# Optimization experiments

Measured on AMD Instinct MI355X. Metric: run time of the kernel, lower is better.

The kernel has to match this reference:

```python
import jax, jax.numpy as jnp
import numpy as np

B, L, D, H = 8, 2048, 1024, 1024
BASE_LR, BASE_WD = 0.01, 0.9


def setup_inputs() -> dict:
    key = jax.random.key(0)
    ks = jax.random.split(key, 8)
    s = 1.0 / np.sqrt(D)
    return {
        "x": jax.random.normal(ks[0], (B, L, D), jnp.float32),
        "hidden": jax.random.normal(ks[1], (B, D, H), jnp.float32),
        "log_base_lr": jnp.array([np.log(BASE_LR)], jnp.float32),
        "w_lr": jax.random.normal(ks[2], (D, 1), jnp.float32) * s,
        "b_lr": jnp.zeros((1,), jnp.float32),
        "log_base_wd": jnp.array([np.log(BASE_WD)], jnp.float32),
        "w_wd": jax.random.normal(ks[3], (D, 1), jnp.float32) * s,
        "b_wd": jnp.zeros((1,), jnp.float32),
        "w_q": jax.random.normal(ks[4], (D, H), jnp.float32) * s,
        "b_q": jnp.zeros((H,), jnp.float32),
        "w_k": jax.random.normal(ks[5], (D, H), jnp.float32) * s,
        "b_k": jnp.zeros((H,), jnp.float32),
        "w_v": jax.random.normal(ks[6], (D, D), jnp.float32) * s,
        "b_v": jnp.zeros((D,), jnp.float32),
    }


def reference(x, hidden, log_base_lr, w_lr, b_lr, log_base_wd, w_wd, b_wd,
              w_q, b_q, w_k, b_k, w_v, b_v):
    batch, length, dim = x.shape
    W_prev = hidden  # [b, d, h]
    query = x @ w_q + b_q                     # [b, l, h]
    key = x @ w_k + b_k                       # [b, l, h]
    value = x @ w_v + b_v                     # [b, l, d]
    lr = jnp.exp(log_base_lr) * jax.nn.sigmoid((x @ w_lr + b_lr)[..., 0])  # [b, l]
    # log(1 - base_wd * sigmoid(.)) via log1p for stability; same math.
    log_wd = jnp.log1p(-jnp.exp(log_base_wd) * jax.nn.sigmoid((x @ w_wd + b_wd)[..., 0]))  # [b, l]
    wd_cross = jnp.exp(jnp.cumsum(log_wd, axis=1))  # [b, l]
    # inner-chunk decay: entry [b, m, l] = exp(sum_{j=m+1..l} log_wd[b, j]) for l >= m
    tri = jnp.triu(jnp.broadcast_to(log_wd[:, None, :], (batch, length, length)), k=1)
    wd_inner = jnp.triu(jnp.exp(jnp.cumsum(tri, axis=2)))  # [b, l, l]
    kq = jnp.einsum('bld,bmd->blm', key, query)            # [b, l, m]
    mask_kq = kq * wd_inner
    WpK_V = jnp.einsum('bdh,blh->bld', W_prev, key) - value  # [b, l, d]
    y_inner = -jnp.einsum('bld,bl,blm->bmd', WpK_V, lr, mask_kq)
    y_cross = jnp.einsum('bdh,blh,bl->bld', W_prev, query, wd_cross)
    y = y_inner + y_cross
    W_next_inner = -jnp.einsum('bld,bl,blh->bdh', WpK_V, lr * wd_inner[:, :, -1], key)
    W_next_cross = W_prev * wd_cross[:, -1][:, None, None]
    W_next = W_next_inner + W_next_cross
    return y, W_next
```

## Files before the change

### kernel.cpp

```cpp
#include <hip/hip_runtime.h>
#include <stdint.h>

#define BB 8
#define LL 2048
#define DD 1024
#define HH 1024
#define BL (BB*LL)

typedef __attribute__((ext_vector_type(8))) short short8;
typedef __attribute__((ext_vector_type(4))) float f32x4;

__device__ __forceinline__ unsigned short f2bf(float f) {
  unsigned int x = __float_as_uint(f);
  unsigned int r = (x + 0x7fffu + ((x >> 16) & 1u)) >> 16;
  return (unsigned short)r;
}
__device__ __forceinline__ float bf2f(unsigned short u) {
  return __uint_as_float(((unsigned int)u) << 16);
}

__device__ __forceinline__ void stage16(const unsigned short* g, unsigned short* l) {
  __builtin_amdgcn_global_load_lds((const __attribute__((address_space(1))) void*)g,
                                   (__attribute__((address_space(3))) void*)l,
                                   16, 0, 0);
}

struct __align__(16) Smem8 {
  unsigned short a[2][16384];
  unsigned short b[2][16384];
};
static_assert(sizeof(Smem8) == 131072, "LDS size");

__device__ __forceinline__ void acc_init8(f32x4 (&acc)[8][4]) {
#pragma unroll
  for (int i = 0; i < 8; ++i)
#pragma unroll
    for (int j = 0; j < 4; ++j)
      acc[i][j] = (f32x4){0.f, 0.f, 0.f, 0.f};
}

template<class FA, class FB>
__device__ __forceinline__ void gemm8_core(FA srcA, FB srcB, int NK,
                                           Smem8* sm, f32x4 (&acc)[8][4]) {
  const int lane = threadIdx.x & 63;
  const int wave = threadIdx.x >> 6;
  const int srow = lane >> 3;
  const int scol = ((lane & 7) ^ srow) * 8;
  const int fk = (lane >> 4) * 8;
  const int fr = lane & 15;
  const int fx = fr & 7;
  const int mwr = (wave >> 2) * 128;
  const int nwr = (wave & 3) * 64;
  const int cA0 = (wave < 4) ? 2 * wave : 2 * wave + 8;
  const int cA1 = cA0 + 8;
  const int cB0 = (wave >> 1) * 8 + 2 * (wave & 1);
  const int cB1 = cB0 + 4;

  auto SA = [&](int p, int kt, int c) {
    stage16(srcA(c * 8 + srow, kt) + scol, &sm->a[p][c * 512]);
    stage16(srcA(c * 8 + 8 + srow, kt) + scol, &sm->a[p][(c + 1) * 512]);
  };
  auto SB = [&](int p, int kt, int c) {
    stage16(srcB(c * 8 + srow, kt) + scol, &sm->b[p][c * 512]);
    stage16(srcB(c * 8 + 8 + srow, kt) + scol, &sm->b[p][(c + 1) * 512]);
  };
  const int kc0 = (((fk >> 3) ^ fx) << 3);
  const int kc1 = ((((32 + fk) >> 3) ^ fx) << 3);

  short8 af[4], bfv[4][2];
  auto LDBk = [&](int p, int kk, int kc) {
#pragma unroll
    for (int j = 0; j < 4; ++j)
      bfv[j][kk] = *(const short8*)&sm->b[p][(nwr + j * 16 + fr) * 64 + kc];
  };
  auto LDA4 = [&](int p, int ih, int kc) {
#pragma unroll
    for (int i = 0; i < 4; ++i)
      af[i] = *(const short8*)&sm->a[p][(mwr + ih * 64 + i * 16 + fr) * 64 + kc];
  };
  auto MMk = [&](int ih, int kk) {
#pragma unroll
    for (int i = 0; i < 4; ++i)
#pragma unroll
      for (int j = 0; j < 4; ++j)
        acc[ih * 4 + i][j] = __builtin_amdgcn_mfma_f32_16x16x32_bf16(
            af[i], bfv[j][kk], acc[ih * 4 + i][j], 0, 0, 0);
  };

#define SCB  __builtin_amdgcn_sched_barrier(0)
#define BARB __builtin_amdgcn_s_barrier()
#define LGKM0 do { asm volatile("s_waitcnt lgkmcnt(0)" ::: "memory"); SCB; } while (0)

  SA(0, 0, cA0); SA(0, 0, cA1); SB(0, 0, cB0); SB(0, 0, cB1);
  asm volatile("s_waitcnt vmcnt(0)" ::: "memory");
  SCB; BARB; SCB;

  for (int t = 0; t < NK; ++t) {
    const int p = t & 1, po = p ^ 1;
    const bool s1 = (t + 1 < NK);
    LDA4(p, 0, kc0); LDBk(p, 0, kc0);
    if (s1) { SA(po, t + 1, cA0); SA(po, t + 1, cA1); }
    SCB; BARB; LGKM0;
    __builtin_amdgcn_s_setprio(1); MMk(0, 0); __builtin_amdgcn_s_setprio(0);
    SCB; BARB; SCB;
    LDA4(p, 1, kc0);
    if (s1) { SB(po, t + 1, cB0); SB(po, t + 1, cB1); }
    SCB; BARB; LGKM0;
    __builtin_amdgcn_s_setprio(1); MMk(1, 0); __builtin_amdgcn_s_setprio(0);
    SCB; BARB; SCB;
    LDA4(p, 0, kc1); LDBk(p, 1, kc1);
    SCB; BARB; LGKM0;
    __builtin_amdgcn_s_setprio(1); MMk(0, 1); __builtin_amdgcn_s_setprio(0);
    SCB; BARB; SCB;
    LDA4(p, 1, kc1);
    SCB; BARB; LGKM0;
    __builtin_amdgcn_s_setprio(1); MMk(1, 1); __builtin_amdgcn_s_setprio(0);
    SCB;
    if (s1) { asm volatile("s_waitcnt vmcnt(0)" ::: "memory"); }
    SCB; BARB; SCB;
  }
#undef LGKM0
#undef BARB
#undef SCB
}

template<typename F>
__device__ __forceinline__ void epi8(const f32x4 (&acc)[8][4], F body) {
  const int lane = threadIdx.x & 63;
  const int wave = threadIdx.x >> 6;
  const int mwr = (wave >> 2) * 128, nwr = (wave & 3) * 64;
#pragma unroll
  for (int i = 0; i < 8; ++i)
#pragma unroll
    for (int j = 0; j < 4; ++j)
#pragma unroll
      for (int jj = 0; jj < 4; ++jj)
        body(mwr + i * 16 + ((lane >> 4) << 2) + jj,
             nwr + j * 16 + (lane & 15), acc[i][j][jj]);
}


__global__ void k_prep_x(const float* __restrict__ x, const float* __restrict__ wlr,
                         const float* __restrict__ wwd, unsigned short* __restrict__ xb,
                         float* __restrict__ lrlog, float* __restrict__ wdlog) {
  const int wave = threadIdx.x >> 6, lane = threadIdx.x & 63;
  const int row = blockIdx.x * 4 + wave;
  const float* xr = x + (size_t)row * DD;
  float s1 = 0.f, s2 = 0.f;
#pragma unroll
  for (int ch = 0; ch < 4; ++ch) {
    const int col = ch * 256 + lane * 4;
    float4 v = *(const float4*)(xr + col);
    float4 a = *(const float4*)(wlr + col);
    float4 b = *(const float4*)(wwd + col);
    s1 += v.x*a.x + v.y*a.y + v.z*a.z + v.w*a.w;
    s2 += v.x*b.x + v.y*b.y + v.z*b.z + v.w*b.w;
    uint2 u;
    u.x = (unsigned)f2bf(v.x) | ((unsigned)f2bf(v.y) << 16);
    u.y = (unsigned)f2bf(v.z) | ((unsigned)f2bf(v.w) << 16);
    *(uint2*)(xb + (size_t)row * DD + col) = u;
  }
#pragma unroll
  for (int off = 32; off > 0; off >>= 1) {
    s1 += __shfl_down(s1, off);
    s2 += __shfl_down(s2, off);
  }
  if (lane == 0) { lrlog[row] = s1; wdlog[row] = s2; }
}

__global__ void k_prep_w(const float* __restrict__ wq, const float* __restrict__ wk,
                         const float* __restrict__ wv, unsigned short* __restrict__ wqt,
                         unsigned short* __restrict__ wkt, unsigned short* __restrict__ wvtn,
                         unsigned short* __restrict__ wkr) {
  const int idx = blockIdx.x * 256 + threadIdx.x;
  if (blockIdx.z == 3) { wkr[idx] = f2bf(wk[idx]); return; }
  const int k = idx >> 10, n = idx & 1023;
  const float* src = (blockIdx.z == 0) ? wq : (blockIdx.z == 1) ? wk : wv;
  unsigned short* dst = (blockIdx.z == 0) ? wqt : (blockIdx.z == 1) ? wkt : wvtn;
  float v = src[(size_t)k * 1024 + n];
  if (blockIdx.z == 2) v = -v;
  dst[(size_t)n * 1024 + k] = f2bf(v);
}

__global__ void k_prep_h(const float* __restrict__ hid, unsigned short* __restrict__ wpb) {
  const size_t i = ((size_t)blockIdx.x * 256 + threadIdx.x) * 4;
  float4 v = *(const float4*)(hid + i);
  uint2 u;
  u.x = (unsigned)f2bf(v.x) | ((unsigned)f2bf(v.y) << 16);
  u.y = (unsigned)f2bf(v.z) | ((unsigned)f2bf(v.w) << 16);
  *(uint2*)(wpb + i) = u;
}

__global__ void k_bias2(const unsigned short* __restrict__ wpb, const float* __restrict__ bk,
                        const float* __restrict__ bv, float* __restrict__ bias2) {
  const int wave = threadIdx.x >> 6, lane = threadIdx.x & 63;
  const int row = blockIdx.x * 4 + wave;
  const unsigned short* wr = wpb + (size_t)row * HH;
  float s = 0.f;
#pragma unroll
  for (int ch = 0; ch < 4; ++ch) {
    const int col = ch * 256 + lane * 4;
    float4 a = *(const float4*)(bk + col);
    ushort4 u = *(const ushort4*)(wr + col);
    s += a.x * bf2f(u.x) + a.y * bf2f(u.y) + a.z * bf2f(u.z) + a.w * bf2f(u.w);
  }
#pragma unroll
  for (int off = 32; off > 0; off >>= 1) s += __shfl_down(s, off);
  if (lane == 0) bias2[row] = s - bv[row & 1023];
}

__global__ void k_scan(const float* __restrict__ lrlog, const float* __restrict__ wdlog,
                       const float* __restrict__ lbl, const float* __restrict__ blr,
                       const float* __restrict__ lbw, const float* __restrict__ bwd,
                       float* __restrict__ lr, float* __restrict__ c,
                       float* __restrict__ s, float* __restrict__ ecl) {
  const int b = blockIdx.x, t = threadIdx.x;
  __shared__ float sums[256];
  const float elr = expf(lbl[0]);
  const float ewd = expf(lbw[0]);
  const float blr0 = blr[0], bwd0 = bwd[0];
  float lw[8];
  const float* wb = wdlog + (size_t)b * LL + t * 8;
  float tot = 0.f;
#pragma unroll
  for (int i = 0; i < 8; ++i) {
    float z = wb[i] + bwd0;
    float sig = 1.f / (1.f + expf(-z));
    tot += log1pf(-ewd * sig);
    lw[i] = tot;
  }
  sums[t] = tot;
  __syncthreads();
  for (int off = 1; off < 256; off <<= 1) {
    float v = (t >= off) ? sums[t - off] : 0.f;
    __syncthreads();
    sums[t] += v;
    __syncthreads();
  }
  const float prev = (t > 0) ? sums[t - 1] : 0.f;
  const float ctot = sums[255];
  const float* lb = lrlog + (size_t)b * LL + t * 8;
#pragma unroll
  for (int i = 0; i < 8; ++i) {
    const int idx = b * LL + t * 8 + i;
    const float ci = prev + lw[i];
    c[idx] = ci;
    float zl = lb[i] + blr0;
    float lri = elr / (1.f + expf(-zl));
    lr[idx] = lri;
    s[idx] = lri * expf(ctot - ci);
  }
  if (t == 0) ecl[b] = expf(ctot);
}


__global__ __launch_bounds__(512, 2) void k8_gemm_m2(const unsigned short* __restrict__ wpb,
    const unsigned short* __restrict__ wkr, const unsigned short* __restrict__ wvtn,
    unsigned short* __restrict__ w2t) {
  __shared__ Smem8 sm;
  const int b = blockIdx.x;
  const int mt = blockIdx.y & 3, nt = blockIdx.y >> 2;
  const int m0 = mt * 256, n0 = nt * 256;
  f32x4 acc[8][4]; acc_init8(acc);
  gemm8_core(
    [&](int r, int kt) { return wpb + (size_t)b * DD * HH + (size_t)(m0 + r) * HH + kt * 64; },
    [&](int r, int kt) { return wkr + (size_t)(n0 + r) * HH + kt * 64; },
    HH / 64, &sm, acc);
  epi8(acc, [&](int rr, int cc, float av) {
    const size_t gi = (size_t)(m0 + rr) * DD + (n0 + cc);
    w2t[(size_t)b * DD * DD + gi] = f2bf(av + bf2f(wvtn[gi]));
  });
}

__global__ __launch_bounds__(512, 2) void k8_gemm_q(const unsigned short* __restrict__ xb,
    const unsigned short* __restrict__ wt, const float* __restrict__ bias,
    const float* __restrict__ c, unsigned short* __restrict__ outb,
    unsigned short* __restrict__ q2b) {
  __shared__ Smem8 sm;
  const int mt = blockIdx.x * 8 + (blockIdx.y & 7);
  const int nt = blockIdx.y >> 3;
  const int m0 = mt * 256, n0 = nt * 256;
  f32x4 acc[8][4]; acc_init8(acc);
  gemm8_core(
    [&](int r, int kt) { return xb + (size_t)(m0 + r) * DD + kt * 64; },
    [&](int r, int kt) { return wt + (size_t)(n0 + r) * DD + kt * 64; },
    DD / 64, &sm, acc);
  const int lane = threadIdx.x & 63, wave = threadIdx.x >> 6;
  const int mwr = (wave >> 2) * 128, nwr = (wave & 3) * 64;
  float er[8][4];
#pragma unroll
  for (int i = 0; i < 8; ++i)
#pragma unroll
    for (int jj = 0; jj < 4; ++jj)
      er[i][jj] = __expf(c[m0 + mwr + i * 16 + ((lane >> 4) << 2) + jj]);
#pragma unroll
  for (int i = 0; i < 8; ++i)
#pragma unroll
    for (int j = 0; j < 4; ++j)
#pragma unroll
      for (int jj = 0; jj < 4; ++jj) {
        const int row = m0 + mwr + i * 16 + ((lane >> 4) << 2) + jj;
        const int col = n0 + nwr + j * 16 + (lane & 15);
        const float v = acc[i][j][jj] + bias[col];
        outb[(size_t)row * HH + col] = f2bf(v);
        q2b[(size_t)row * HH + col] = f2bf(v * er[i][jj]);
      }
}

__global__ __launch_bounds__(512, 2) void k8_gemm_k(const unsigned short* __restrict__ xb,
    const unsigned short* __restrict__ wt, const float* __restrict__ bias,
    const float* __restrict__ s, unsigned short* __restrict__ kb,
    unsigned short* __restrict__ k2t) {
  __shared__ Smem8 sm;
  const int mt = blockIdx.x * 8 + (blockIdx.y & 7);
  const int nt = blockIdx.y >> 3;
  const int m0 = mt * 256, n0 = nt * 256;
  f32x4 acc[8][4]; acc_init8(acc);
  gemm8_core(
    [&](int r, int kt) { return xb + (size_t)(m0 + r) * DD + kt * 64; },
    [&](int r, int kt) { return wt + (size_t)(n0 + r) * DD + kt * 64; },
    DD / 64, &sm, acc);
  const int lane = threadIdx.x & 63, wave = threadIdx.x >> 6;
  const int mwr = (wave >> 2) * 128, nwr = (wave & 3) * 64;
#pragma unroll
  for (int i = 0; i < 8; ++i)
#pragma unroll
    for (int j = 0; j < 4; ++j) {
      const int col = n0 + nwr + j * 16 + (lane & 15);
      const float bias_c = bias[col];
      const int row0 = m0 + mwr + i * 16 + ((lane >> 4) << 2);
      const int b = row0 >> 11, ml0 = row0 & 2047;
      unsigned short tmp[4];
#pragma unroll
      for (int jj = 0; jj < 4; ++jj) {
        float v = acc[i][j][jj] + bias_c;
        kb[(size_t)(row0 + jj) * HH + col] = f2bf(v);
        tmp[jj] = f2bf(v * s[row0 + jj]);
      }
      uint2 u;
      u.x = (unsigned)tmp[0] | ((unsigned)tmp[1] << 16);
      u.y = (unsigned)tmp[2] | ((unsigned)tmp[3] << 16);
      *(uint2*)&k2t[((size_t)b * HH + col) * LL + ml0] = u;
    }
}

__global__ __launch_bounds__(512, 2) void k8_gemm_u(const unsigned short* __restrict__ xb,
    const unsigned short* __restrict__ w2t, const float* __restrict__ bias2,
    unsigned short* __restrict__ ut) {
  __shared__ Smem8 sm;
  const int b = blockIdx.x;
  const int mt = blockIdx.x * 8 + (blockIdx.y & 7);
  const int nt = blockIdx.y >> 3;
  const int m0 = mt * 256, n0 = nt * 256;
  f32x4 acc[8][4]; acc_init8(acc);
  gemm8_core(
    [&](int r, int kt) { return xb + (size_t)(m0 + r) * DD + kt * 64; },
    [&](int r, int kt) { return w2t + (size_t)b * DD * DD + (size_t)(n0 + r) * DD + kt * 64; },
    DD / 64, &sm, acc);
  const int lane = threadIdx.x & 63, wave = threadIdx.x >> 6;
  const int mwr = (wave >> 2) * 128, nwr = (wave & 3) * 64;
#pragma unroll
  for (int i = 0; i < 8; ++i)
#pragma unroll
    for (int j = 0; j < 4; ++j) {
      const int col = n0 + nwr + j * 16 + (lane & 15);
      const float b2c = bias2[b * DD + col];
      const int row0 = m0 + mwr + i * 16 + ((lane >> 4) << 2);
      const int ml0 = row0 & 2047;
      unsigned short tmp[4];
#pragma unroll
      for (int jj = 0; jj < 4; ++jj) tmp[jj] = f2bf(acc[i][j][jj] + b2c);
      uint2 u;
      u.x = (unsigned)tmp[0] | ((unsigned)tmp[1] << 16);
      u.y = (unsigned)tmp[2] | ((unsigned)tmp[3] << 16);
      *(uint2*)&ut[((size_t)b * DD + col) * LL + ml0] = u;
    }
}

__global__ __launch_bounds__(512, 2) void k8_gemm_p(const unsigned short* __restrict__ qb,
    const unsigned short* __restrict__ kb, const float* __restrict__ lr,
    const float* __restrict__ c, unsigned short* __restrict__ pb) {
  __shared__ Smem8 sm;
  const int b = blockIdx.x;
  const int t = blockIdx.y;
  int mt = (int)((sqrtf(8.f * (float)t + 1.f) - 1.f) * 0.5f);
  while ((mt + 1) * (mt + 2) / 2 <= t) ++mt;
  while (mt * (mt + 1) / 2 > t) --mt;
  const int nt = t - mt * (mt + 1) / 2;
  const int base = b * LL;
  const int m0 = mt * 256, n0 = nt * 256;
  f32x4 acc[8][4]; acc_init8(acc);
  gemm8_core(
    [&](int rr, int kt) { return qb + (size_t)(base + m0 + rr) * HH + kt * 64; },
    [&](int rr, int kt) { return kb + (size_t)(base + n0 + rr) * HH + kt * 64; },
    HH / 64, &sm, acc);
  const int lane = threadIdx.x & 63, wave = threadIdx.x >> 6;
  const int mwr = (wave >> 2) * 128, nwr = (wave & 3) * 64;
  if (nt != mt) {
    const float cref = c[base + m0];
    float er[8][4], fc[4];
#pragma unroll
    for (int i = 0; i < 8; ++i)
#pragma unroll
      for (int jj = 0; jj < 4; ++jj)
        er[i][jj] = __expf(c[base + m0 + mwr + i * 16 + ((lane >> 4) << 2) + jj] - cref);
#pragma unroll
    for (int j = 0; j < 4; ++j) {
      const int l = n0 + nwr + j * 16 + (lane & 15);
      fc[j] = lr[base + l] * __expf(cref - c[base + l]);
    }
#pragma unroll
    for (int i = 0; i < 8; ++i)
#pragma unroll
      for (int j = 0; j < 4; ++j) {
        const int l = n0 + nwr + j * 16 + (lane & 15);
        const int row0 = m0 + mwr + i * 16 + ((lane >> 4) << 2);
#pragma unroll
        for (int jj = 0; jj < 4; ++jj) {
          const float v = -acc[i][j][jj] * er[i][jj] * fc[j];
          pb[((size_t)base + row0 + jj) * LL + l] = f2bf(v);
        }
      }
  } else {
    epi8(acc, [&](int rr, int cc, float av) {
      const int m = m0 + rr, l = n0 + cc;
      float v = 0.f;
      if (l <= m) v = -av * lr[base + l] * __expf(c[base + m] - c[base + l]);
      pb[((size_t)base + m) * LL + l] = f2bf(v);
    });
  }
}

__global__ __launch_bounds__(512, 2) void k8_gemm_y(const unsigned short* __restrict__ pb,
    const unsigned short* __restrict__ ut, const unsigned short* __restrict__ q2b,
    const unsigned short* __restrict__ wpb, float* __restrict__ out) {
  __shared__ Smem8 sm;
  const int b = blockIdx.x;
  const int mt = blockIdx.y & 7;
  const int nt = blockIdx.y >> 3;
  const int m0 = mt * 256, n0 = nt * 256;
  const int NK1 = (mt + 1) * 4;
  f32x4 acc[8][4]; acc_init8(acc);
  gemm8_core(
    [&](int r, int kt) {
      return (kt < NK1) ? pb + (size_t)b * LL * LL + (size_t)(m0 + r) * LL + kt * 64
                        : q2b + ((size_t)b * LL + m0 + r) * HH + (kt - NK1) * 64;
    },
    [&](int r, int kt) {
      return (kt < NK1) ? ut + (size_t)b * DD * LL + (size_t)(n0 + r) * LL + kt * 64
                        : wpb + (size_t)b * DD * HH + (size_t)(n0 + r) * HH + (kt - NK1) * 64;
    },
    NK1 + 16, &sm, acc);
  epi8(acc, [&](int rr, int cc, float av) {
    out[((size_t)b * LL + m0 + rr) * DD + (n0 + cc)] = av;
  });
}

__global__ __launch_bounds__(512, 2) void k8_gemm_wn(const unsigned short* __restrict__ ut,
    const unsigned short* __restrict__ k2t, const float* __restrict__ hid,
    const float* __restrict__ ecl, float* __restrict__ out2) {
  __shared__ Smem8 sm;
  const int b = blockIdx.x;
  const int mt = blockIdx.y & 3, nt = blockIdx.y >> 2;
  const int m0 = mt * 256, n0 = nt * 256;
  f32x4 acc[8][4]; acc_init8(acc);
  gemm8_core(
    [&](int r, int kt) { return ut + (size_t)b * DD * LL + (size_t)(m0 + r) * LL + kt * 64; },
    [&](int r, int kt) { return k2t + (size_t)b * HH * LL + (size_t)(n0 + r) * LL + kt * 64; },
    LL / 64, &sm, acc);
  const float eclb = ecl[b];
  epi8(acc, [&](int rr, int cc, float av) {
    const size_t gi = ((size_t)b * DD + (m0 + rr)) * HH + (n0 + cc);
    out2[gi] = -av + eclb * hid[gi];
  });
}


extern "C" void kernel_launch(void* const* d_in, const int* in_sizes, int n_in,
                              void* d_out, int out_size, void* d_ws, size_t ws_size,
                              hipStream_t stream) {
  (void)in_sizes; (void)n_in; (void)out_size; (void)ws_size;
  const float* x   = (const float*)d_in[0];
  const float* hid = (const float*)d_in[1];
  const float* lbl = (const float*)d_in[2];
  const float* wlr = (const float*)d_in[3];
  const float* blr = (const float*)d_in[4];
  const float* lbw = (const float*)d_in[5];
  const float* wwd = (const float*)d_in[6];
  const float* bwd = (const float*)d_in[7];
  const float* wq  = (const float*)d_in[8];
  const float* bq  = (const float*)d_in[9];
  const float* wk  = (const float*)d_in[10];
  const float* bk  = (const float*)d_in[11];
  const float* wv  = (const float*)d_in[12];
  const float* bv  = (const float*)d_in[13];
  float* out = (float*)d_out;

  char* w = (char*)d_ws;
  constexpr size_t SZ_XB  = (size_t)BL * DD * 2;
  constexpr size_t SZ_QB  = (size_t)BL * HH * 2;
  constexpr size_t SZ_KB  = (size_t)BL * HH * 2;
  constexpr size_t SZ_K2T = (size_t)BB * HH * LL * 2;
  constexpr size_t SZ_UT  = (size_t)BB * DD * LL * 2;
  constexpr size_t SZ_PB  = (size_t)BB * LL * LL * 2;
  constexpr size_t SZ_WT  = (size_t)DD * HH * 2;
  constexpr size_t SZ_WPB = (size_t)BB * DD * HH * 2;
  constexpr size_t SZ_V16 = (size_t)BL * 4;

  size_t off = 0;
  unsigned short* xb   = (unsigned short*)(w + off); off += SZ_XB;
  unsigned short* qb   = (unsigned short*)(w + off); off += SZ_QB;
  unsigned short* kb   = (unsigned short*)(w + off); off += SZ_KB;
  unsigned short* k2t  = (unsigned short*)(w + off); off += SZ_K2T;
  unsigned short* ut   = (unsigned short*)(w + off); off += SZ_UT;
  unsigned short* pb   = (unsigned short*)(w + off); off += SZ_PB;
  unsigned short* wqt  = (unsigned short*)(w + off); off += SZ_WT;
  unsigned short* wkt  = (unsigned short*)(w + off); off += SZ_WT;
  unsigned short* wvtn = (unsigned short*)(w + off); off += SZ_WT;
  unsigned short* wpb  = (unsigned short*)(w + off); off += SZ_WPB;
  float* lrlog = (float*)(w + off); off += SZ_V16;
  float* wdlog = (float*)(w + off); off += SZ_V16;
  float* lr    = (float*)(w + off); off += SZ_V16;
  float* c     = (float*)(w + off); off += SZ_V16;
  float* s     = (float*)(w + off); off += SZ_V16;
  float* ecl   = (float*)(w + off); off += 256;
  float* bias2 = (float*)(w + off); off += (size_t)BB * DD * 4;

  unsigned short* w2t = pb;
  unsigned short* wkr = pb + (size_t)BB * DD * DD;

  unsigned short* q2b = (unsigned short*)(out + (size_t)BL * DD);
  float* out2 = out + (size_t)BL * DD;

  k_prep_x<<<dim3(BL / 4), 256, 0, stream>>>(x, wlr, wwd, xb, lrlog, wdlog);
  k_prep_w<<<dim3(4096, 1, 4), 256, 0, stream>>>(wq, wk, wv, wqt, wkt, wvtn, wkr);
  k_prep_h<<<dim3((unsigned)((size_t)BB * DD * HH / 1024)), 256, 0, stream>>>(hid, wpb);
  k_scan<<<dim3(BB), 256, 0, stream>>>(lrlog, wdlog, lbl, blr, lbw, bwd, lr, c, s, ecl);
  k_bias2<<<dim3(BB * DD / 4), 256, 0, stream>>>(wpb, bk, bv, bias2);

  k8_gemm_m2<<<dim3(8, 16), 512, 0, stream>>>(wpb, wkr, wvtn, w2t);
  k8_gemm_q<<<dim3(8, 32), 512, 0, stream>>>(xb, wqt, bq, c, qb, q2b);
  k8_gemm_k<<<dim3(8, 32), 512, 0, stream>>>(xb, wkt, bk, s, kb, k2t);
  k8_gemm_u<<<dim3(8, 32), 512, 0, stream>>>(xb, w2t, bias2, ut);
  k8_gemm_p<<<dim3(8, 36), 512, 0, stream>>>(qb, kb, lr, c, pb);
  k8_gemm_y<<<dim3(8, 32), 512, 0, stream>>>(pb, ut, q2b, wpb, out);
  k8_gemm_wn<<<dim3(8, 16), 512, 0, stream>>>(ut, k2t, hid, ecl, out2);
}
```

Before: 636.2 us.

## Restructure GEMM core pipeline, shrink tiles for small GEMMs, balance causal y GEMM

Rewrites the shared GEMM mainloop to prefetch B two stages ahead with fewer barriers and partial lgkmcnt waits, so LDS loads overlap MFMA work. Adds a half-height tile variant (128 rows) for the m2 and wn GEMMs, doubling their block count to fill more CUs. Load-balances the causal y GEMM by pairing row tile sr with 7-sr in each block, splitting the K range and accumulating into a pre-zeroed output with float atomics. This adds a zeroing pass and atomic traffic on the output and makes the result order nondeterministic.

```diff
diff --git a/kernel.cpp b/kernel.cpp
--- a/kernel.cpp
+++ b/kernel.cpp
@@ -25,23 +25,26 @@
                                    16, 0, 0);
 }
 
-struct __align__(16) Smem8 {
-  unsigned short a[2][16384];
+template<int MI>
+struct __align__(16) SmemT {
+  unsigned short a[2][MI*2048];
   unsigned short b[2][16384];
 };
-static_assert(sizeof(Smem8) == 131072, "LDS size");
-
-__device__ __forceinline__ void acc_init8(f32x4 (&acc)[8][4]) {
-#pragma unroll
-  for (int i = 0; i < 8; ++i)
+
+template<int MI>
+__device__ __forceinline__ void acc_initT(f32x4 (&acc)[MI][4]) {
+#pragma unroll
+  for (int i = 0; i < MI; ++i)
 #pragma unroll
     for (int j = 0; j < 4; ++j)
       acc[i][j] = (f32x4){0.f, 0.f, 0.f, 0.f};
 }
 
-template<class FA, class FB>
-__device__ __forceinline__ void gemm8_core(FA srcA, FB srcB, int NK,
-                                           Smem8* sm, f32x4 (&acc)[8][4]) {
+#define SCB __builtin_amdgcn_sched_barrier(0)
+
+template<int MI, class FA, class FB>
+__device__ __forceinline__ void gemm9_core(FA srcA, FB srcB, int NK,
+                                           SmemT<MI>* sm, f32x4 (&acc)[MI][4]) {
   const int lane = threadIdx.x & 63;
   const int wave = threadIdx.x >> 6;
   const int srow = lane >> 3;
@@ -49,88 +52,103 @@
   const int fk = (lane >> 4) * 8;
   const int fr = lane & 15;
   const int fx = fr & 7;
-  const int mwr = (wave >> 2) * 128;
+  const int mwr = (wave >> 2) * (MI * 16);
   const int nwr = (wave & 3) * 64;
-  const int cA0 = (wave < 4) ? 2 * wave : 2 * wave + 8;
+  const int cA0 = (MI == 8) ? ((wave < 4) ? 2 * wave : 2 * wave + 8) : 2 * wave;
   const int cA1 = cA0 + 8;
   const int cB0 = (wave >> 1) * 8 + 2 * (wave & 1);
   const int cB1 = cB0 + 4;
-
-  auto SA = [&](int p, int kt, int c) {
+  const int kc0 = (((fk >> 3) ^ fx) << 3);
+  const int kc1 = ((((32 + fk) >> 3) ^ fx) << 3);
+
+  auto SA2 = [&](int p, int kt, int c) {
     stage16(srcA(c * 8 + srow, kt) + scol, &sm->a[p][c * 512]);
     stage16(srcA(c * 8 + 8 + srow, kt) + scol, &sm->a[p][(c + 1) * 512]);
   };
-  auto SB = [&](int p, int kt, int c) {
+  auto SB2 = [&](int p, int kt, int c) {
     stage16(srcB(c * 8 + srow, kt) + scol, &sm->b[p][c * 512]);
     stage16(srcB(c * 8 + 8 + srow, kt) + scol, &sm->b[p][(c + 1) * 512]);
   };
-  const int kc0 = (((fk >> 3) ^ fx) << 3);
-  const int kc1 = ((((32 + fk) >> 3) ^ fx) << 3);
-
-  short8 af[4], bfv[4][2];
-  auto LDBk = [&](int p, int kk, int kc) {
+
+  short8 af0[4], af1[4], bfv[4][2];
+  auto LDB4 = [&](int p, int kk, int kc) {
 #pragma unroll
     for (int j = 0; j < 4; ++j)
       bfv[j][kk] = *(const short8*)&sm->b[p][(nwr + j * 16 + fr) * 64 + kc];
   };
-  auto LDA4 = [&](int p, int ih, int kc) {
+  auto LDA4 = [&](short8 (&dst)[4], int p, int iho, int kc) {
 #pragma unroll
     for (int i = 0; i < 4; ++i)
-      af[i] = *(const short8*)&sm->a[p][(mwr + ih * 64 + i * 16 + fr) * 64 + kc];
+      dst[i] = *(const short8*)&sm->a[p][(mwr + iho + i * 16 + fr) * 64 + kc];
   };
-  auto MMk = [&](int ih, int kk) {
+  auto MM16 = [&](short8 (&a4)[4], int accb, int kk) {
 #pragma unroll
     for (int i = 0; i < 4; ++i)
 #pragma unroll
       for (int j = 0; j < 4; ++j)
-        acc[ih * 4 + i][j] = __builtin_amdgcn_mfma_f32_16x16x32_bf16(
-            af[i], bfv[j][kk], acc[ih * 4 + i][j], 0, 0, 0);
+        acc[accb + i][j] = __builtin_amdgcn_mfma_f32_16x16x32_bf16(
+            a4[i], bfv[j][kk], acc[accb + i][j], 0, 0, 0);
   };
 
-#define SCB  __builtin_amdgcn_sched_barrier(0)
-#define BARB __builtin_amdgcn_s_barrier()
-#define LGKM0 do { asm volatile("s_waitcnt lgkmcnt(0)" ::: "memory"); SCB; } while (0)
-
-  SA(0, 0, cA0); SA(0, 0, cA1); SB(0, 0, cB0); SB(0, 0, cB1);
-  asm volatile("s_waitcnt vmcnt(0)" ::: "memory");
-  SCB; BARB; SCB;
+  SA2(0, 0, cA0);
+  if (MI == 8) SA2(0, 0, cA1);
+  SB2(0, 0, cB0); SB2(0, 0, cB1);
+  if (NK > 1) {
+    SB2(1, 1, cB0); SB2(1, 1, cB1);
+    asm volatile("s_waitcnt vmcnt(4)" ::: "memory");
+  } else {
+    asm volatile("s_waitcnt vmcnt(0)" ::: "memory");
+  }
+  SCB; __builtin_amdgcn_s_barrier(); SCB;
 
   for (int t = 0; t < NK; ++t) {
     const int p = t & 1, po = p ^ 1;
-    const bool s1 = (t + 1 < NK);
-    LDA4(p, 0, kc0); LDBk(p, 0, kc0);
-    if (s1) { SA(po, t + 1, cA0); SA(po, t + 1, cA1); }
-    SCB; BARB; LGKM0;
-    __builtin_amdgcn_s_setprio(1); MMk(0, 0); __builtin_amdgcn_s_setprio(0);
-    SCB; BARB; SCB;
-    LDA4(p, 1, kc0);
-    if (s1) { SB(po, t + 1, cB0); SB(po, t + 1, cB1); }
-    SCB; BARB; LGKM0;
-    __builtin_amdgcn_s_setprio(1); MMk(1, 0); __builtin_amdgcn_s_setprio(0);
-    SCB; BARB; SCB;
-    LDA4(p, 0, kc1); LDBk(p, 1, kc1);
-    SCB; BARB; LGKM0;
-    __builtin_amdgcn_s_setprio(1); MMk(0, 1); __builtin_amdgcn_s_setprio(0);
-    SCB; BARB; SCB;
-    LDA4(p, 1, kc1);
-    SCB; BARB; LGKM0;
-    __builtin_amdgcn_s_setprio(1); MMk(1, 1); __builtin_amdgcn_s_setprio(0);
-    SCB;
-    if (s1) { asm volatile("s_waitcnt vmcnt(0)" ::: "memory"); }
-    SCB; BARB; SCB;
-  }
-#undef LGKM0
-#undef BARB
-#undef SCB
-}
-
-template<typename F>
-__device__ __forceinline__ void epi8(const f32x4 (&acc)[8][4], F body) {
+    const bool s1 = (t + 1 < NK), s2 = (t + 2 < NK);
+    if (s1) { SA2(po, t + 1, cA0); if (MI == 8) SA2(po, t + 1, cA1); }
+    if constexpr (MI == 8) {
+      LDB4(p, 0, kc0);
+      LDA4(af0, p, 0, kc0);
+      LDA4(af1, p, 64, kc0);
+      asm volatile("s_waitcnt lgkmcnt(4)" ::: "memory"); SCB;
+      __builtin_amdgcn_s_setprio(1); MM16(af0, 0, 0); __builtin_amdgcn_s_setprio(0);
+      LDB4(p, 1, kc1);
+      LDA4(af0, p, 0, kc1);
+      asm volatile("s_waitcnt lgkmcnt(8)" ::: "memory"); SCB;
+      __builtin_amdgcn_s_setprio(1); MM16(af1, 4, 0); __builtin_amdgcn_s_setprio(0);
+      LDA4(af1, p, 64, kc1);
+      asm volatile("s_waitcnt lgkmcnt(4)" ::: "memory"); SCB;
+      __builtin_amdgcn_s_setprio(1); MM16(af0, 0, 1); __builtin_amdgcn_s_setprio(0);
+      SCB; __builtin_amdgcn_s_barrier(); SCB;
+      if (s2) { SB2(p, t + 2, cB0); SB2(p, t + 2, cB1); }
+      asm volatile("s_waitcnt lgkmcnt(0)" ::: "memory"); SCB;
+      __builtin_amdgcn_s_setprio(1); MM16(af1, 4, 1); __builtin_amdgcn_s_setprio(0);
+      SCB;
+    } else {
+      LDB4(p, 0, kc0);
+      LDA4(af0, p, 0, kc0);
+      LDB4(p, 1, kc1);
+      LDA4(af1, p, 0, kc1);
+      asm volatile("s_waitcnt lgkmcnt(8)" ::: "memory"); SCB;
+      __builtin_amdgcn_s_setprio(1); MM16(af0, 0, 0); __builtin_amdgcn_s_setprio(0);
+      asm volatile("s_waitcnt lgkmcnt(0)" ::: "memory"); SCB;
+      SCB; __builtin_amdgcn_s_barrier(); SCB;
+      if (s2) { SB2(p, t + 2, cB0); SB2(p, t + 2, cB1); }
+      __builtin_amdgcn_s_setprio(1); MM16(af1, 0, 1); __builtin_amdgcn_s_setprio(0);
+      SCB;
+    }
+    if (s2)      { asm volatile("s_waitcnt vmcnt(4)" ::: "memory"); }
+    else if (s1) { asm volatile("s_waitcnt vmcnt(0)" ::: "memory"); }
+    SCB; __builtin_amdgcn_s_barrier(); SCB;
+  }
+}
+
+template<int MI, typename F>
+__device__ __forceinline__ void epiT(const f32x4 (&acc)[MI][4], F body) {
   const int lane = threadIdx.x & 63;
   const int wave = threadIdx.x >> 6;
-  const int mwr = (wave >> 2) * 128, nwr = (wave & 3) * 64;
-#pragma unroll
-  for (int i = 0; i < 8; ++i)
+  const int mwr = (wave >> 2) * (MI * 16), nwr = (wave & 3) * 64;
+#pragma unroll
+  for (int i = 0; i < MI; ++i)
 #pragma unroll
     for (int j = 0; j < 4; ++j)
 #pragma unroll
@@ -139,6 +157,10 @@
              nwr + j * 16 + (lane & 15), acc[i][j][jj]);
 }
 
+
+__global__ void k_zero(float4* __restrict__ p) {
+  p[(size_t)blockIdx.x * 256 + threadIdx.x] = make_float4(0.f, 0.f, 0.f, 0.f);
+}
 
 __global__ void k_prep_x(const float* __restrict__ x, const float* __restrict__ wlr,
                          const float* __restrict__ wwd, unsigned short* __restrict__ xb,
@@ -254,34 +276,34 @@
 }
 
 
-__global__ __launch_bounds__(512, 2) void k8_gemm_m2(const unsigned short* __restrict__ wpb,
+__global__ __launch_bounds__(512, 2) void k9_gemm_m2(const unsigned short* __restrict__ wpb,
     const unsigned short* __restrict__ wkr, const unsigned short* __restrict__ wvtn,
     unsigned short* __restrict__ w2t) {
-  __shared__ Smem8 sm;
+  __shared__ SmemT<4> sm;
   const int b = blockIdx.x;
-  const int mt = blockIdx.y & 3, nt = blockIdx.y >> 2;
-  const int m0 = mt * 256, n0 = nt * 256;
-  f32x4 acc[8][4]; acc_init8(acc);
-  gemm8_core(
+  const int mt = blockIdx.y & 7, nt = blockIdx.y >> 3;
+  const int m0 = mt * 128, n0 = nt * 256;
+  f32x4 acc[4][4]; acc_initT<4>(acc);
+  gemm9_core<4>(
     [&](int r, int kt) { return wpb + (size_t)b * DD * HH + (size_t)(m0 + r) * HH + kt * 64; },
     [&](int r, int kt) { return wkr + (size_t)(n0 + r) * HH + kt * 64; },
     HH / 64, &sm, acc);
-  epi8(acc, [&](int rr, int cc, float av) {
+  epiT<4>(acc, [&](int rr, int cc, float av) {
     const size_t gi = (size_t)(m0 + rr) * DD + (n0 + cc);
     w2t[(size_t)b * DD * DD + gi] = f2bf(av + bf2f(wvtn[gi]));
   });
 }
 
-__global__ __launch_bounds__(512, 2) void k8_gemm_q(const unsigned short* __restrict__ xb,
+__global__ __launch_bounds__(512, 2) void k9_gemm_q(const unsigned short* __restrict__ xb,
     const unsigned short* __restrict__ wt, const float* __restrict__ bias,
     const float* __restrict__ c, unsigned short* __restrict__ outb,
     unsigned short* __restrict__ q2b) {
-  __shared__ Smem8 sm;
+  __shared__ SmemT<8> sm;
   const int mt = blockIdx.x * 8 + (blockIdx.y & 7);
   const int nt = blockIdx.y >> 3;
   const int m0 = mt * 256, n0 = nt * 256;
-  f32x4 acc[8][4]; acc_init8(acc);
-  gemm8_core(
+  f32x4 acc[8][4]; acc_initT<8>(acc);
+  gemm9_core<8>(
     [&](int r, int kt) { return xb + (size_t)(m0 + r) * DD + kt * 64; },
     [&](int r, int kt) { return wt + (size_t)(n0 + r) * DD + kt * 64; },
     DD / 64, &sm, acc);
@@ -307,16 +329,16 @@
       }
 }
 
-__global__ __launch_bounds__(512, 2) void k8_gemm_k(const unsigned short* __restrict__ xb,
+__global__ __launch_bounds__(512, 2) void k9_gemm_k(const unsigned short* __restrict__ xb,
     const unsigned short* __restrict__ wt, const float* __restrict__ bias,
     const float* __restrict__ s, unsigned short* __restrict__ kb,
     unsigned short* __restrict__ k2t) {
-  __shared__ Smem8 sm;
+  __shared__ SmemT<8> sm;
   const int mt = blockIdx.x * 8 + (blockIdx.y & 7);
   const int nt = blockIdx.y >> 3;
   const int m0 = mt * 256, n0 = nt * 256;
-  f32x4 acc[8][4]; acc_init8(acc);
-  gemm8_core(
+  f32x4 acc[8][4]; acc_initT<8>(acc);
+  gemm9_core<8>(
     [&](int r, int kt) { return xb + (size_t)(m0 + r) * DD + kt * 64; },
     [&](int r, int kt) { return wt + (size_t)(n0 + r) * DD + kt * 64; },
     DD / 64, &sm, acc);
@@ -344,16 +366,16 @@
     }
 }
 
-__global__ __launch_bounds__(512, 2) void k8_gemm_u(const unsigned short* __restrict__ xb,
+__global__ __launch_bounds__(512, 2) void k9_gemm_u(const unsigned short* __restrict__ xb,
     const unsigned short* __restrict__ w2t, const float* __restrict__ bias2,
     unsigned short* __restrict__ ut) {
-  __shared__ Smem8 sm;
+  __shared__ SmemT<8> sm;
   const int b = blockIdx.x;
   const int mt = blockIdx.x * 8 + (blockIdx.y & 7);
   const int nt = blockIdx.y >> 3;
   const int m0 = mt * 256, n0 = nt * 256;
-  f32x4 acc[8][4]; acc_init8(acc);
-  gemm8_core(
+  f32x4 acc[8][4]; acc_initT<8>(acc);
+  gemm9_core<8>(
     [&](int r, int kt) { return xb + (size_t)(m0 + r) * DD + kt * 64; },
     [&](int r, int kt) { return w2t + (size_t)b * DD * DD + (size_t)(n0 + r) * DD + kt * 64; },
     DD / 64, &sm, acc);
@@ -377,10 +399,10 @@
     }
 }
 
-__global__ __launch_bounds__(512, 2) void k8_gemm_p(const unsigned short* __restrict__ qb,
+__global__ __launch_bounds__(512, 2) void k9_gemm_p(const unsigned short* __restrict__ qb,
     const unsigned short* __restrict__ kb, const float* __restrict__ lr,
     const float* __restrict__ c, unsigned short* __restrict__ pb) {
-  __shared__ Smem8 sm;
+  __shared__ SmemT<8> sm;
   const int b = blockIdx.x;
   const int t = blockIdx.y;
   int mt = (int)((sqrtf(8.f * (float)t + 1.f) - 1.f) * 0.5f);
@@ -389,8 +411,8 @@
   const int nt = t - mt * (mt + 1) / 2;
   const int base = b * LL;
   const int m0 = mt * 256, n0 = nt * 256;
-  f32x4 acc[8][4]; acc_init8(acc);
-  gemm8_core(
+  f32x4 acc[8][4]; acc_initT<8>(acc);
+  gemm9_core<8>(
     [&](int rr, int kt) { return qb + (size_t)(base + m0 + rr) * HH + kt * 64; },
     [&](int rr, int kt) { return kb + (size_t)(base + n0 + rr) * HH + kt * 64; },
     HH / 64, &sm, acc);
@@ -422,7 +444,7 @@
         }
       }
   } else {
-    epi8(acc, [&](int rr, int cc, float av) {
+    epiT<8>(acc, [&](int rr, int cc, float av) {
       const int m = m0 + rr, l = n0 + cc;
       float v = 0.f;
       if (l <= m) v = -av * lr[base + l] * __expf(c[base + m] - c[base + l]);
@@ -431,45 +453,56 @@
   }
 }
 
-__global__ __launch_bounds__(512, 2) void k8_gemm_y(const unsigned short* __restrict__ pb,
+__global__ __launch_bounds__(512, 2) void k9_gemm_y(const unsigned short* __restrict__ pb,
     const unsigned short* __restrict__ ut, const unsigned short* __restrict__ q2b,
     const unsigned short* __restrict__ wpb, float* __restrict__ out) {
-  __shared__ Smem8 sm;
+  __shared__ SmemT<8> sm;
   const int b = blockIdx.x;
-  const int mt = blockIdx.y & 7;
-  const int nt = blockIdx.y >> 3;
-  const int m0 = mt * 256, n0 = nt * 256;
-  const int NK1 = (mt + 1) * 4;
-  f32x4 acc[8][4]; acc_init8(acc);
-  gemm8_core(
-    [&](int r, int kt) {
-      return (kt < NK1) ? pb + (size_t)b * LL * LL + (size_t)(m0 + r) * LL + kt * 64
-                        : q2b + ((size_t)b * LL + m0 + r) * HH + (kt - NK1) * 64;
-    },
-    [&](int r, int kt) {
-      return (kt < NK1) ? ut + (size_t)b * DD * LL + (size_t)(n0 + r) * LL + kt * 64
-                        : wpb + (size_t)b * DD * HH + (size_t)(n0 + r) * HH + (kt - NK1) * 64;
-    },
-    NK1 + 16, &sm, acc);
-  epi8(acc, [&](int rr, int cc, float av) {
-    out[((size_t)b * LL + m0 + rr) * DD + (n0 + cc)] = av;
-  });
-}
-
-__global__ __launch_bounds__(512, 2) void k8_gemm_wn(const unsigned short* __restrict__ ut,
+  const int sr = blockIdx.y & 7, nt = blockIdx.y >> 3;
+  const int n0 = nt * 256;
+  const unsigned short* pbB = pb + (size_t)b * LL * LL;
+  const unsigned short* utB = ut + (size_t)b * DD * LL;
+  const unsigned short* q2B = q2b + (size_t)b * LL * HH;
+  const unsigned short* wpB = wpb + (size_t)b * DD * HH;
+  f32x4 acc[8][4];
+#pragma unroll
+  for (int job = 0; job < 2; ++job) {
+    const int mt = job ? (7 - sr) : sr;
+    const int m0 = mt * 256;
+    const int H = (mt + 1) * 2;
+    const int pk0 = job ? H : 0;
+    const int qk0 = job ? 8 : 0;
+    acc_initT<8>(acc);
+    gemm9_core<8>(
+      [&](int r, int kt) { return pbB + (size_t)(m0 + r) * LL + (pk0 + kt) * 64; },
+      [&](int r, int kt) { return utB + (size_t)(n0 + r) * LL + (pk0 + kt) * 64; },
+      H, &sm, acc);
+    gemm9_core<8>(
+      [&](int r, int kt) { return q2B + (size_t)(m0 + r) * HH + (qk0 + kt) * 64; },
+      [&](int r, int kt) { return wpB + (size_t)(n0 + r) * HH + (qk0 + kt) * 64; },
+      8, &sm, acc);
+    epiT<8>(acc, [&](int rr, int cc, float av) {
+      unsafeAtomicAdd(&out[((size_t)b * LL + m0 + rr) * DD + (n0 + cc)], av);
+    });
+    asm volatile("s_waitcnt vmcnt(0)" ::: "memory");
+    SCB;
+  }
+}
+
+__global__ __launch_bounds__(512, 2) void k9_gemm_wn(const unsigned short* __restrict__ ut,
     const unsigned short* __restrict__ k2t, const float* __restrict__ hid,
     const float* __restrict__ ecl, float* __restrict__ out2) {
-  __shared__ Smem8 sm;
+  __shared__ SmemT<4> sm;
   const int b = blockIdx.x;
-  const int mt = blockIdx.y & 3, nt = blockIdx.y >> 2;
-  const int m0 = mt * 256, n0 = nt * 256;
-  f32x4 acc[8][4]; acc_init8(acc);
-  gemm8_core(
+  const int mt = blockIdx.y & 7, nt = blockIdx.y >> 3;
+  const int m0 = mt * 128, n0 = nt * 256;
+  f32x4 acc[4][4]; acc_initT<4>(acc);
+  gemm9_core<4>(
     [&](int r, int kt) { return ut + (size_t)b * DD * LL + (size_t)(m0 + r) * LL + kt * 64; },
     [&](int r, int kt) { return k2t + (size_t)b * HH * LL + (size_t)(n0 + r) * LL + kt * 64; },
     LL / 64, &sm, acc);
   const float eclb = ecl[b];
-  epi8(acc, [&](int rr, int cc, float av) {
+  epiT<4>(acc, [&](int rr, int cc, float av) {
     const size_t gi = ((size_t)b * DD + (m0 + rr)) * HH + (n0 + cc);
     out2[gi] = -av + eclb * hid[gi];
   });
@@ -532,17 +565,18 @@
   unsigned short* q2b = (unsigned short*)(out + (size_t)BL * DD);
   float* out2 = out + (size_t)BL * DD;
 
+  k_zero<<<dim3(BL * DD / 4 / 256), 256, 0, stream>>>((float4*)out);
   k_prep_x<<<dim3(BL / 4), 256, 0, stream>>>(x, wlr, wwd, xb, lrlog, wdlog);
   k_prep_w<<<dim3(4096, 1, 4), 256, 0, stream>>>(wq, wk, wv, wqt, wkt, wvtn, wkr);
   k_prep_h<<<dim3((unsigned)((size_t)BB * DD * HH / 1024)), 256, 0, stream>>>(hid, wpb);
   k_scan<<<dim3(BB), 256, 0, stream>>>(lrlog, wdlog, lbl, blr, lbw, bwd, lr, c, s, ecl);
   k_bias2<<<dim3(BB * DD / 4), 256, 0, stream>>>(wpb, bk, bv, bias2);
 
-  k8_gemm_m2<<<dim3(8, 16), 512, 0, stream>>>(wpb, wkr, wvtn, w2t);
-  k8_gemm_q<<<dim3(8, 32), 512, 0, stream>>>(xb, wqt, bq, c, qb, q2b);
-  k8_gemm_k<<<dim3(8, 32), 512, 0, stream>>>(xb, wkt, bk, s, kb, k2t);
-  k8_gemm_u<<<dim3(8, 32), 512, 0, stream>>>(xb, w2t, bias2, ut);
-  k8_gemm_p<<<dim3(8, 36), 512, 0, stream>>>(qb, kb, lr, c, pb);
-  k8_gemm_y<<<dim3(8, 32), 512, 0, stream>>>(pb, ut, q2b, wpb, out);
-  k8_gemm_wn<<<dim3(8, 16), 512, 0, stream>>>(ut, k2t, hid, ecl, out2);
-}
+  k9_gemm_m2<<<dim3(8, 32), 512, 0, stream>>>(wpb, wkr, wvtn, w2t);
+  k9_gemm_q<<<dim3(8, 32), 512, 0, stream>>>(xb, wqt, bq, c, qb, q2b);
+  k9_gemm_k<<<dim3(8, 32), 512, 0, stream>>>(xb, wkt, bk, s, kb, k2t);
+  k9_gemm_u<<<dim3(8, 32), 512, 0, stream>>>(xb, w2t, bias2, ut);
+  k9_gemm_p<<<dim3(8, 36), 512, 0, stream>>>(qb, kb, lr, c, pb);
+  k9_gemm_y<<<dim3(8, 32), 512, 0, stream>>>(pb, ut, q2b, wpb, out);
+  k9_gemm_wn<<<dim3(8, 32), 512, 0, stream>>>(ut, k2t, hid, ecl, out2);
+}
```

Measured after the change: 675.1 us. 6.1% more time.
